# Kernel optimization log

Measured on AMD Instinct MI355X. Metric: run time of the kernel, lower is better.

The kernel has to match this reference:

```python
import jax, jax.numpy as jnp
from jax import lax
import numpy as np

B, T, C, N = 64, 1024, 1, 128  # batch, max seq len, num_conjugates, num_tags


def setup_inputs() -> dict:
    key = jax.random.key(0)
    ks = jax.random.split(key, 6)
    emissions = jax.random.normal(ks[0], (B, T, C, N), dtype=jnp.float32)
    token_sizes = jax.random.randint(ks[1], (B,), T // 2, T + 1)  # ragged lengths in [512, 1024]
    targets = jax.random.randint(ks[2], (B, T), 0, N)
    transitions = jax.random.normal(ks[3], (1, C, N, N), dtype=jnp.float32) * 0.1
    head_transitions = jax.random.normal(ks[4], (1, C, N), dtype=jnp.float32) * 0.1
    last_transitions = jax.random.normal(ks[5], (1, C, N), dtype=jnp.float32) * 0.1
    return dict(emissions=emissions, token_sizes=token_sizes, targets=targets,
                transitions=transitions, head_transitions=head_transitions,
                last_transitions=last_transitions)


def _crf(emissions, token_sizes, targets, transitions, head_transitions, last_transitions):
    # emissions: [B, T, C, N] padded; token_sizes: [B]; targets: [B, T]
    Bq, Tq, Cq, Nq = emissions.shape
    trans = transitions[0]          # [C, N, N]
    head = head_transitions[0]      # [C, N]
    last = last_transitions[0]      # [C, N]

    # ---- log partition (Log semiring forward algorithm; same math as the
    # log-depth semiring tree reduction in crf_partition) ----
    alpha0 = head[None, :, :] + emissions[:, 0]            # [B, C, N]
    emits = jnp.moveaxis(emissions[:, 1:], 1, 0)           # [T-1, B, C, N]
    valid = jnp.arange(1, Tq)[:, None] < token_sizes[None, :]  # [T-1, B]

    def step(alpha, inp):
        emit_t, v = inp
        # alpha[b,c,i] + trans[c,i,j] -> logsumexp over i
        new = jax.nn.logsumexp(alpha[:, :, :, None] + trans[None], axis=2) + emit_t
        return jnp.where(v[:, None, None], new, alpha), None

    alphaT, _ = lax.scan(step, alpha0, (emits, valid))
    log_partitions = jax.nn.logsumexp(alphaT + last[None, :, :], axis=-1)  # [B, C]

    # ---- path score (crf_segment_reduce with Log semiring) ----
    emit_sel = jnp.take_along_axis(emissions, targets[:, :, None, None], axis=3)[..., 0]  # [B, T, C]
    mask = (jnp.arange(Tq)[None, :] < token_sizes[:, None]).astype(emissions.dtype)       # [B, T]
    emit_sum = jnp.sum(emit_sel * mask[:, :, None], axis=1)                               # [B, C]

    prev_t, curr_t = targets[:, :-1], targets[:, 1:]
    trans_sel = trans[:, prev_t, curr_t]                                                  # [C, B, T-1]
    mask2 = (jnp.arange(1, Tq)[None, :] < token_sizes[:, None]).astype(emissions.dtype)   # [B, T-1]
    trans_sum = jnp.sum(trans_sel * mask2[None], axis=-1)                                 # [C, B]

    head_sel = head[:, targets[:, 0]]                                                     # [C, B]
    last_tag = jnp.take_along_axis(targets, (token_sizes - 1)[:, None], axis=1)[:, 0]     # [B]
    last_sel = last[:, last_tag]                                                          # [C, B]

    log_scores = emit_sum + trans_sum.T + head_sel.T + last_sel.T                         # [B, C]
    return jnp.stack([log_partitions, log_scores])  # [2, B, C]


def reference(emissions, token_sizes, targets, transitions, head_transitions, last_transitions):
    return _crf(emissions, token_sizes, targets, transitions, head_transitions, last_transitions)
```

## Files before the change

### kernel.cpp

```cpp
#include <hip/hip_runtime.h>
#include <math.h>

#define Bq 64
#define Tq 1024
#define Nq 128
#define SEG 129
#define NFW (SEG - 1)
#define NBW (SEG - 1)
#define WPC 16
#define LN2 0.6931471805599453f

typedef __attribute__((ext_vector_type(8))) _Float16 half8;
typedef __attribute__((ext_vector_type(2))) _Float16 h2;
typedef __attribute__((ext_vector_type(4))) float f32x4;

union BU { int u[4]; int4 v; half8 h; };
union E8 { int2 v; h2 p[2]; };
union E16 { int2 v2[2]; half8 h; };

__device__ __forceinline__ int pk16(float a, float b) {
    auto p = __builtin_amdgcn_cvt_pkrtz(a, b);
    return *(int*)&p;
}

__device__ __forceinline__ int MMAP(int q, int g, int j) {
    return 16 * (2 * q + (j >> 2)) + 4 * g + (j & 3);
}

__global__ __launch_bounds__(256)
void crf_prep_kernel(const float* __restrict__ em,
                     const float* __restrict__ trans,
                     const int* __restrict__ token_sizes,
                     const int* __restrict__ targets,
                     const float* __restrict__ head,
                     const float* __restrict__ last,
                     _Float16* __restrict__ eeh,
                     int4* __restrict__ aF, int4* __restrict__ aB,
                     float* __restrict__ out) {
    const int bid = blockIdx.x;
    const int tid = threadIdx.x;
    if (bid < 4096) {
        const size_t i = ((size_t)bid * 256 + tid) * 8;
        const float4* src = (const float4*)(em + i);
        float4 x0 = src[0], x1 = src[1];
        BU r;
        r.u[0] = pk16(__expf(x0.x), __expf(x0.y));
        r.u[1] = pk16(__expf(x0.z), __expf(x0.w));
        r.u[2] = pk16(__expf(x1.x), __expf(x1.y));
        r.u[3] = pk16(__expf(x1.z), __expf(x1.w));
        *(int4*)(eeh + i) = r.v;
        return;
    }
    if (bid < 4112) {
        const int fb = bid - 4096;
        const bool fwd = (fb < 8);
        const int kf = (fb & 7) * 4 + (tid >> 6);
        const int L = tid & 63;
        const int c = L & 15, g = L >> 4;
        const int r = kf >> 2, q = kf & 3;
        BU v;
        #pragma unroll
        for (int j = 0; j < 8; ++j) {
            const int m = MMAP(q, g, j);
            const int n = 16 * r + c;
            const float tv = fwd ? trans[m * Nq + n] : trans[n * Nq + m];
            v.h[j] = (_Float16)__expf(tv);
        }
        (fwd ? aF : aB)[kf * 64 + L] = v.v;
        return;
    }
    {
        const int b = bid - 4112;
        const int tsz = token_sizes[b];
        const int* tg = targets + b * Tq;
        const float* emc = em + (size_t)b * Tq * Nq;
        float sc = 0.f;
        for (int t = tid; t < tsz; t += 256) {
            int cur = tg[t];
            sc += emc[(size_t)t * Nq + cur];
            if (t >= 1) sc += trans[tg[t - 1] * Nq + cur];
        }
        #pragma unroll
        for (int off = 32; off >= 1; off >>= 1)
            sc += __shfl_xor(sc, off, 64);
        __shared__ float wsum[4];
        if ((tid & 63) == 0) wsum[tid >> 6] = sc;
        __syncthreads();
        if (tid == 0) {
            float tot = (wsum[0] + wsum[1]) + (wsum[2] + wsum[3]);
            out[Bq + b] = tot + head[tg[0]] + last[tg[tsz - 1]];
        }
    }
}

__device__ __forceinline__ void fwd_step(
    int k, int lenc, int lo, int hi, int g,
    const _Float16* __restrict__ eeh_c,
    const half8 (&afrag)[32], BU (&bf)[4],
    E8 (&eeCur)[8], E8 (&eeNxt)[8], int& Ecum)
{
    f32x4 acc[8];
    #pragma unroll
    for (int r = 0; r < 8; ++r) {
        f32x4 z = {0.f, 0.f, 0.f, 0.f};
        z = __builtin_amdgcn_mfma_f32_16x16x32_f16(afrag[r*4+0], bf[0].h, z, 0, 0, 0);
        z = __builtin_amdgcn_mfma_f32_16x16x32_f16(afrag[r*4+1], bf[1].h, z, 0, 0, 0);
        z = __builtin_amdgcn_mfma_f32_16x16x32_f16(afrag[r*4+2], bf[2].h, z, 0, 0, 0);
        z = __builtin_amdgcn_mfma_f32_16x16x32_f16(afrag[r*4+3], bf[3].h, z, 0, 0, 0);
        acc[r] = z;
    }
    {
        const int tn = min(lo + k, hi);
        const _Float16* bp = eeh_c + (size_t)tn * Nq;
        #pragma unroll
        for (int r = 0; r < 8; ++r)
            eeNxt[r].v = *(const int2*)(bp + 16*r + 4*g);
    }
    float w[32];
    float mx = 0.f;
    #pragma unroll
    for (int r = 0; r < 8; ++r) {
        #pragma unroll
        for (int i = 0; i < 4; ++i) {
            const float ee = (float)eeCur[r].p[i >> 1][i & 1];
            const float wv = acc[r][i] * ee;
            w[r*4+i] = wv;
            mx = fmaxf(mx, wv);
        }
    }
    mx = fmaxf(mx, __shfl_xor(mx, 16, 64));
    mx = fmaxf(mx, __shfl_xor(mx, 32, 64));
    const int eb = (__float_as_int(mx) >> 23) & 255;
    const float sig = __int_as_float((253 - eb) << 23);
    const bool act = (k <= lenc);
    #pragma unroll
    for (int q = 0; q < 4; ++q) {
        const int n0 = pk16(w[8*q+0]*sig, w[8*q+1]*sig);
        const int n1 = pk16(w[8*q+2]*sig, w[8*q+3]*sig);
        const int n2 = pk16(w[8*q+4]*sig, w[8*q+5]*sig);
        const int n3 = pk16(w[8*q+6]*sig, w[8*q+7]*sig);
        bf[q].u[0] = act ? n0 : bf[q].u[0];
        bf[q].u[1] = act ? n1 : bf[q].u[1];
        bf[q].u[2] = act ? n2 : bf[q].u[2];
        bf[q].u[3] = act ? n3 : bf[q].u[3];
    }
    Ecum += act ? (eb - 126) : 0;
}

__device__ __forceinline__ void bwd_step(
    int k, int lenc, int lo, int hi, int g,
    const _Float16* __restrict__ eeh_c,
    const half8 (&afrag)[32], BU (&bf)[4],
    E16 (&eeCur)[4], E16 (&eeNxt)[4], int& Ecum)
{
    BU beff[4];
    #pragma unroll
    for (int q = 0; q < 4; ++q) beff[q].h = bf[q].h * eeCur[q].h;
    f32x4 acc[8];
    #pragma unroll
    for (int r = 0; r < 8; ++r) {
        f32x4 z = {0.f, 0.f, 0.f, 0.f};
        z = __builtin_amdgcn_mfma_f32_16x16x32_f16(afrag[r*4+0], beff[0].h, z, 0, 0, 0);
        z = __builtin_amdgcn_mfma_f32_16x16x32_f16(afrag[r*4+1], beff[1].h, z, 0, 0, 0);
        z = __builtin_amdgcn_mfma_f32_16x16x32_f16(afrag[r*4+2], beff[2].h, z, 0, 0, 0);
        z = __builtin_amdgcn_mfma_f32_16x16x32_f16(afrag[r*4+3], beff[3].h, z, 0, 0, 0);
        acc[r] = z;
    }
    {
        const int tn = max(hi - k, lo);
        const _Float16* bp = eeh_c + (size_t)tn * Nq;
        #pragma unroll
        for (int q = 0; q < 4; ++q) {
            eeNxt[q].v2[0] = *(const int2*)(bp + 32*q + 4*g);
            eeNxt[q].v2[1] = *(const int2*)(bp + 32*q + 16 + 4*g);
        }
    }
    float mx = 0.f;
    #pragma unroll
    for (int r = 0; r < 8; ++r) {
        #pragma unroll
        for (int i = 0; i < 4; ++i) mx = fmaxf(mx, acc[r][i]);
    }
    mx = fmaxf(mx, __shfl_xor(mx, 16, 64));
    mx = fmaxf(mx, __shfl_xor(mx, 32, 64));
    const int eb = (__float_as_int(mx) >> 23) & 255;
    const float sig = __int_as_float((253 - eb) << 23);
    const bool act = (k <= lenc);
    #pragma unroll
    for (int q = 0; q < 4; ++q) {
        const int n0 = pk16(acc[2*q][0]*sig,   acc[2*q][1]*sig);
        const int n1 = pk16(acc[2*q][2]*sig,   acc[2*q][3]*sig);
        const int n2 = pk16(acc[2*q+1][0]*sig, acc[2*q+1][1]*sig);
        const int n3 = pk16(acc[2*q+1][2]*sig, acc[2*q+1][3]*sig);
        bf[q].u[0] = act ? n0 : bf[q].u[0];
        bf[q].u[1] = act ? n1 : bf[q].u[1];
        bf[q].u[2] = act ? n2 : bf[q].u[2];
        bf[q].u[3] = act ? n3 : bf[q].u[3];
    }
    Ecum += act ? (eb - 126) : 0;
}

__global__ __launch_bounds__(64, 1)
void crf_worker_kernel(const float* __restrict__ emissions,
                       const _Float16* __restrict__ eeh,
                       const int4* __restrict__ aF,
                       const int4* __restrict__ aB,
                       const int* __restrict__ token_sizes,
                       const float* __restrict__ head,
                       const float* __restrict__ last,
                       float* __restrict__ wsA, float* __restrict__ wsB,
                       float* __restrict__ wsLa, float* __restrict__ wsLb) {
    const int L = threadIdx.x;
    const int bid = blockIdx.x;

    const int b = bid >> 4;
    const int wv = bid & 15;
    const bool isFwd = (wv < 8);
    const int half_ = wv & 7;
    const int c = L & 15;
    const int g = L >> 4;
    const int s = (isFwd ? 1 : 2) + 16 * half_ + c;

    const float* em_c = emissions + (size_t)b * Tq * Nq;
    const _Float16* eeh_c = eeh + (size_t)b * Tq * Nq;
    const int tsz = token_sizes[b];
    const int nst = tsz - 1;
    const int base = nst / SEG;
    const int rem = nst % SEG;
    const int lo = 1 + (s - 1) * base + min(s - 1, rem);
    const int lenc = base + ((s <= rem) ? 1 : 0);
    const int hi = lo + lenc - 1;
    const int kmax = base + 1;

    half8 afrag[32];
    {
        const int4* asrc = isFwd ? aF : aB;
        #pragma unroll
        for (int kf = 0; kf < 32; ++kf) {
            BU t; t.v = asrc[kf * 64 + L];
            afrag[kf] = t.h;
        }
    }

    BU bf[4];
    float M0c;
    {
        float a0[32];
        float mx = -1e30f;
        #pragma unroll
        for (int q = 0; q < 4; ++q) {
            #pragma unroll
            for (int j2 = 0; j2 < 8; ++j2) {
                const int m = MMAP(q, g, j2);
                float v;
                if (isFwd) v = (s == 1)   ? (head[m] + em_c[m]) : 0.f;
                else       v = (s == SEG) ? last[m]             : 0.f;
                a0[q*8+j2] = v;
                mx = fmaxf(mx, v);
            }
        }
        mx = fmaxf(mx, __shfl_xor(mx, 16, 64));
        mx = fmaxf(mx, __shfl_xor(mx, 32, 64));
        M0c = mx;
        #pragma unroll
        for (int q = 0; q < 4; ++q) {
            #pragma unroll
            for (int p = 0; p < 4; ++p)
                bf[q].u[p] = pk16(__expf(a0[q*8+2*p]   - M0c),
                                  __expf(a0[q*8+2*p+1] - M0c));
        }
    }

    int Ecum = 0;
    int k = 1;
    if (isFwd) {
        E8 eeA[8], eeB8[8];
        const _Float16* bp = eeh_c + (size_t)lo * Nq;
        #pragma unroll
        for (int r = 0; r < 8; ++r) eeA[r].v = *(const int2*)(bp + 16*r + 4*g);
        for (; k + 1 <= kmax; k += 2) {
            fwd_step(k,   lenc, lo, hi, g, eeh_c, afrag, bf, eeA, eeB8, Ecum);
            fwd_step(k+1, lenc, lo, hi, g, eeh_c, afrag, bf, eeB8, eeA, Ecum);
        }
        if (k <= kmax)
            fwd_step(k, lenc, lo, hi, g, eeh_c, afrag, bf, eeA, eeB8, Ecum);
    } else {
        E16 eeA[4], eeB8[4];
        const _Float16* bp = eeh_c + (size_t)hi * Nq;
        #pragma unroll
        for (int q = 0; q < 4; ++q) {
            eeA[q].v2[0] = *(const int2*)(bp + 32*q + 4*g);
            eeA[q].v2[1] = *(const int2*)(bp + 32*q + 16 + 4*g);
        }
        for (; k + 1 <= kmax; k += 2) {
            bwd_step(k,   lenc, lo, hi, g, eeh_c, afrag, bf, eeA, eeB8, Ecum);
            bwd_step(k+1, lenc, lo, hi, g, eeh_c, afrag, bf, eeB8, eeA, Ecum);
        }
        if (k <= kmax)
            bwd_step(k, lenc, lo, hi, g, eeh_c, afrag, bf, eeA, eeB8, Ecum);
    }

    {
        float* dst = isFwd ? (wsA + ((size_t)(s - 1) * Bq + b) * Nq)
                           : (wsB + ((size_t)(s - 2) * Bq + b) * Nq);
        #pragma unroll
        for (int q = 0; q < 4; ++q) {
            f32x4 v0, v1;
            #pragma unroll
            for (int t = 0; t < 4; ++t) { v0[t] = (float)bf[q].h[t]; v1[t] = (float)bf[q].h[4+t]; }
            *(f32x4*)(dst + 32*q + 4*g)      = v0;
            *(f32x4*)(dst + 32*q + 16 + 4*g) = v1;
        }
        if (g == 0) {
            const float led = M0c + (float)Ecum * LN2;
            if (isFwd) wsLa[(s - 1) * Bq + b] = led;
            else       wsLb[(s - 2) * Bq + b] = led;
        }
    }
}

__global__ __launch_bounds__(512)
void crf_combine_kernel(const float* __restrict__ wsA,
                        const float* __restrict__ wsB,
                        const float* __restrict__ wsLa,
                        const float* __restrict__ wsLb,
                        float* __restrict__ out) {
    const int b = blockIdx.x;
    const int tid = threadIdx.x;
    const int wv = tid >> 6;
    const int l = tid & 63;
    __shared__ float part[8];

    float tot = 0.f;
    for (int s = 2 + wv; s <= SEG - 1; s += 8) {
        const float* bb = wsB + ((size_t)(s - 2) * Bq + b) * Nq;
        const float* aa = wsA + ((size_t)(s - 2) * Bq + b) * Nq;
        float z = bb[l] * aa[l] + bb[l + 64] * aa[l + 64];
        float cc = bb[l] + bb[l + 64];
        #pragma unroll
        for (int off = 32; off >= 1; off >>= 1) {
            z += __shfl_xor(z, off, 64);
            cc += __shfl_xor(cc, off, 64);
        }
        tot += __logf(z) + wsLa[(s - 2) * Bq + b] - __logf(cc);
    }
    if (wv == 0) {
        const float* bb = wsB + ((size_t)(SEG - 2) * Bq + b) * Nq;
        const float* aa = wsA + ((size_t)(SEG - 2) * Bq + b) * Nq;
        float z = bb[l] * aa[l] + bb[l + 64] * aa[l + 64];
        #pragma unroll
        for (int off = 32; off >= 1; off >>= 1)
            z += __shfl_xor(z, off, 64);
        tot += __logf(z) + wsLb[(SEG - 2) * Bq + b] + wsLa[(SEG - 2) * Bq + b];
    }
    if (l == 0) part[wv] = tot;
    __syncthreads();
    if (tid == 0) {
        float tz = 0.f;
        #pragma unroll
        for (int i = 0; i < 8; ++i) tz += part[i];
        out[b] = tz;
    }
}

extern "C" void kernel_launch(void* const* d_in, const int* in_sizes, int n_in,
                              void* d_out, int out_size, void* d_ws, size_t ws_size,
                              hipStream_t stream) {
    const float* emissions   = (const float*)d_in[0];
    const int*   token_sizes = (const int*)d_in[1];
    const int*   targets     = (const int*)d_in[2];
    const float* transitions = (const float*)d_in[3];
    const float* head        = (const float*)d_in[4];
    const float* last        = (const float*)d_in[5];
    float* out = (float*)d_out;

    char* wp = (char*)d_ws;
    _Float16* eeh = (_Float16*)wp;                       wp += (size_t)Bq * Tq * Nq * 2;
    int4* aF = (int4*)wp;                                wp += 32 * 64 * 16;
    int4* aB = (int4*)wp;                                wp += 32 * 64 * 16;
    float* wsA  = (float*)wp;                            wp += (size_t)NFW * Bq * Nq * 4;
    float* wsB  = (float*)wp;                            wp += (size_t)NBW * Bq * Nq * 4;
    float* wsLa = (float*)wp;                            wp += NFW * Bq * 4;
    float* wsLb = (float*)wp;                            wp += NBW * Bq * 4;

    crf_prep_kernel<<<4096 + 16 + Bq, 256, 0, stream>>>(
        emissions, transitions, token_sizes, targets, head, last,
        eeh, aF, aB, out);
    crf_worker_kernel<<<Bq * WPC, 64, 0, stream>>>(
        emissions, eeh, aF, aB, token_sizes, head, last,
        wsA, wsB, wsLa, wsLb);
    crf_combine_kernel<<<Bq, 512, 0, stream>>>(wsA, wsB, wsLa, wsLb, out);
}
```

Baseline: 43.37 us.

## Skip padded emission exp, move path score into worker, parallelize combine with atomics

The prep kernel now skips exponentiating emission rows beyond each sequence's token size. The path-score computation moves from the prep kernel into extra single-wave blocks of the worker kernel, which also zero the partition output. The combine kernel spreads each chain across four blocks that accumulate into the output with atomicAdd. This cuts wasted exp/convert traffic on padding and widens the combine kernel's parallelism, at the cost of float atomics, which make the summation order nondeterministic.

```diff
diff --git a/kernel.cpp b/kernel.cpp
--- a/kernel.cpp
+++ b/kernel.cpp
@@ -31,15 +31,14 @@
 void crf_prep_kernel(const float* __restrict__ em,
                      const float* __restrict__ trans,
                      const int* __restrict__ token_sizes,
-                     const int* __restrict__ targets,
-                     const float* __restrict__ head,
-                     const float* __restrict__ last,
                      _Float16* __restrict__ eeh,
-                     int4* __restrict__ aF, int4* __restrict__ aB,
-                     float* __restrict__ out) {
+                     int4* __restrict__ aF, int4* __restrict__ aB) {
     const int bid = blockIdx.x;
     const int tid = threadIdx.x;
     if (bid < 4096) {
+        const int b = bid >> 6;
+        const int row0 = (bid & 63) * 16;
+        if (row0 >= token_sizes[b]) return;
         const size_t i = ((size_t)bid * 256 + tid) * 8;
         const float4* src = (const float4*)(em + i);
         float4 x0 = src[0], x1 = src[1];
@@ -51,7 +50,7 @@
         *(int4*)(eeh + i) = r.v;
         return;
     }
-    if (bid < 4112) {
+    {
         const int fb = bid - 4096;
         const bool fwd = (fb < 8);
         const int kf = (fb & 7) * 4 + (tid >> 6);
@@ -67,29 +66,6 @@
             v.h[j] = (_Float16)__expf(tv);
         }
         (fwd ? aF : aB)[kf * 64 + L] = v.v;
-        return;
-    }
-    {
-        const int b = bid - 4112;
-        const int tsz = token_sizes[b];
-        const int* tg = targets + b * Tq;
-        const float* emc = em + (size_t)b * Tq * Nq;
-        float sc = 0.f;
-        for (int t = tid; t < tsz; t += 256) {
-            int cur = tg[t];
-            sc += emc[(size_t)t * Nq + cur];
-            if (t >= 1) sc += trans[tg[t - 1] * Nq + cur];
-        }
-        #pragma unroll
-        for (int off = 32; off >= 1; off >>= 1)
-            sc += __shfl_xor(sc, off, 64);
-        __shared__ float wsum[4];
-        if ((tid & 63) == 0) wsum[tid >> 6] = sc;
-        __syncthreads();
-        if (tid == 0) {
-            float tot = (wsum[0] + wsum[1]) + (wsum[2] + wsum[3]);
-            out[Bq + b] = tot + head[tg[0]] + last[tg[tsz - 1]];
-        }
     }
 }
 
@@ -206,12 +182,36 @@
                        const int4* __restrict__ aF,
                        const int4* __restrict__ aB,
                        const int* __restrict__ token_sizes,
+                       const int* __restrict__ targets,
+                       const float* __restrict__ transitions,
                        const float* __restrict__ head,
                        const float* __restrict__ last,
                        float* __restrict__ wsA, float* __restrict__ wsB,
-                       float* __restrict__ wsLa, float* __restrict__ wsLb) {
+                       float* __restrict__ wsLa, float* __restrict__ wsLb,
+                       float* __restrict__ out) {
     const int L = threadIdx.x;
     const int bid = blockIdx.x;
+
+    if (bid >= Bq * WPC) {
+        const int b = bid - Bq * WPC;
+        const int tsz = token_sizes[b];
+        const int* tg = targets + b * Tq;
+        const float* emc = emissions + (size_t)b * Tq * Nq;
+        float sc = 0.f;
+        for (int t = L; t < tsz; t += 64) {
+            int cur = tg[t];
+            sc += emc[(size_t)t * Nq + cur];
+            if (t >= 1) sc += transitions[tg[t - 1] * Nq + cur];
+        }
+        #pragma unroll
+        for (int off = 32; off >= 1; off >>= 1)
+            sc += __shfl_xor(sc, off, 64);
+        if (L == 0) {
+            out[Bq + b] = sc + head[tg[0]] + last[tg[tsz - 1]];
+            out[b] = 0.0f;
+        }
+        return;
+    }
 
     const int b = bid >> 4;
     const int wv = bid & 15;
@@ -325,42 +325,29 @@
                         const float* __restrict__ wsLa,
                         const float* __restrict__ wsLb,
                         float* __restrict__ out) {
-    const int b = blockIdx.x;
-    const int tid = threadIdx.x;
-    const int wv = tid >> 6;
-    const int l = tid & 63;
-    __shared__ float part[8];
+    const int chain = blockIdx.x >> 2;
+    const int sub = blockIdx.x & 3;
+    const int wq = sub * 8 + (threadIdx.x >> 6);
+    const int l = threadIdx.x & 63;
 
     float tot = 0.f;
-    for (int s = 2 + wv; s <= SEG - 1; s += 8) {
-        const float* bb = wsB + ((size_t)(s - 2) * Bq + b) * Nq;
-        const float* aa = wsA + ((size_t)(s - 2) * Bq + b) * Nq;
+    #pragma unroll
+    for (int rep = 0; rep < 4; ++rep) {
+        const int j = wq + 32 * rep;
+        const float* bb = wsB + ((size_t)j * Bq + chain) * Nq;
+        const float* aa = wsA + ((size_t)j * Bq + chain) * Nq;
         float z = bb[l] * aa[l] + bb[l + 64] * aa[l + 64];
         float cc = bb[l] + bb[l + 64];
         #pragma unroll
         for (int off = 32; off >= 1; off >>= 1) {
-            z += __shfl_xor(z, off, 64);
+            z  += __shfl_xor(z, off, 64);
             cc += __shfl_xor(cc, off, 64);
         }
-        tot += __logf(z) + wsLa[(s - 2) * Bq + b] - __logf(cc);
-    }
-    if (wv == 0) {
-        const float* bb = wsB + ((size_t)(SEG - 2) * Bq + b) * Nq;
-        const float* aa = wsA + ((size_t)(SEG - 2) * Bq + b) * Nq;
-        float z = bb[l] * aa[l] + bb[l + 64] * aa[l + 64];
-        #pragma unroll
-        for (int off = 32; off >= 1; off >>= 1)
-            z += __shfl_xor(z, off, 64);
-        tot += __logf(z) + wsLb[(SEG - 2) * Bq + b] + wsLa[(SEG - 2) * Bq + b];
-    }
-    if (l == 0) part[wv] = tot;
-    __syncthreads();
-    if (tid == 0) {
-        float tz = 0.f;
-        #pragma unroll
-        for (int i = 0; i < 8; ++i) tz += part[i];
-        out[b] = tz;
-    }
+        float term = __logf(z) + wsLa[j * Bq + chain];
+        term += (j == NFW - 1) ? wsLb[(NBW - 1) * Bq + chain] : -__logf(cc);
+        tot += term;
+    }
+    if (l == 0) atomicAdd(&out[chain], tot);
 }
 
 extern "C" void kernel_launch(void* const* d_in, const int* in_sizes, int n_in,
@@ -383,11 +370,10 @@
     float* wsLa = (float*)wp;                            wp += NFW * Bq * 4;
     float* wsLb = (float*)wp;                            wp += NBW * Bq * 4;
 
-    crf_prep_kernel<<<4096 + 16 + Bq, 256, 0, stream>>>(
-        emissions, transitions, token_sizes, targets, head, last,
-        eeh, aF, aB, out);
-    crf_worker_kernel<<<Bq * WPC, 64, 0, stream>>>(
-        emissions, eeh, aF, aB, token_sizes, head, last,
-        wsA, wsB, wsLa, wsLb);
-    crf_combine_kernel<<<Bq, 512, 0, stream>>>(wsA, wsB, wsLa, wsLb, out);
-}
+    crf_prep_kernel<<<4096 + 16, 256, 0, stream>>>(
+        emissions, transitions, token_sizes, eeh, aF, aB);
+    crf_worker_kernel<<<Bq * WPC + Bq, 64, 0, stream>>>(
+        emissions, eeh, aF, aB, token_sizes, targets, transitions, head, last,
+        wsA, wsB, wsLa, wsLb, out);
+    crf_combine_kernel<<<4 * Bq, 512, 0, stream>>>(wsA, wsB, wsLa, wsLb, out);
+}
```

New measurement: 53.01 us. +22.2%, slower.
